# Kernel optimization log

Measured on AMD Instinct MI355X. Metric: run time of the kernel, lower is better.

Reference implementation:

```python
import jax, jax.numpy as jnp
import numpy as np
from jax import lax

S = 512          # IMAGE_SIZE
NP = 11          # num parts (num_layers)
B = 4            # batch_size (hard-coded in original)
FEAT = 9 * 126 * 126  # fc1 in-features: 9*(((S-4)//2-2)//2)**2

_DRAW_ORDER_BIAS = [
    [0.848048096156426, -0.5299192642332049, -0.06623990802915061, 0.5299192642332049, 0.848048096156426, 0.10600601201955324],
    [0.9986295347545738, 0.05233595624294379, -0.001158806553435294, -0.05233595624294379, 0.9986295347545738, -0.022375972781727708],
    [0.8290375725550417, -0.5591929034707469, 0.2758348051438573, 0.5591929034707469, 0.8290375725550417, -0.3679706692738145],
    [0.898794046299167, -0.4383711467890774, -0.1455594743327377, 0.4383711467890774, 0.898794046299167, -0.0037996949408528533],
    [0.7431448254773944, -0.6691306063588581, -0.04191544748895007, 0.6691306063588581, 0.7431448254773944, -0.4385935274816633],
    [0.984807753012208, 0.17364817766693036, 0.09489218227886641, -0.17364817766693036, 0.984807753012208, 0.204382434413116],
    [0.754709580222772, 0.6560590289905073, 0.34755260971666235, -0.6560590289905073, 0.754709580222772, 0.3941816342013059],
    [0.992546151641322, 0.12186934340514749, 0.2294707093902736, -0.12186934340514749, 0.992546151641322, 0.42009272589950425],
    [0.766044443118978, 0.6427876096865394, 0.3722248189351549, -0.6427876096865394, 0.766044443118978, -0.02028262460152125],
    [0.9993908270190958, -0.03489949670250096, -0.16002611816129286, 0.03489949670250096, 0.9993908270190958, 0.3825967914560618],
    [0.9961946980917455, 0.08715574274765818, -0.2047079583082938, -0.08715574274765818, 0.9961946980917455, 0.15872754699051406],
]
CANON_BIAS = np.asarray(_DRAW_ORDER_BIAS, dtype=np.float32).reshape(-1)  # [66]


def setup_inputs() -> dict:
    key = jax.random.key(0)
    ks = jax.random.split(key, 8)
    x = jax.random.uniform(ks[0], (B, (NP + 1) * S, S, 4), dtype=jnp.float32)
    return {
        "x": x,
        "conv1_w": jax.random.normal(ks[1], (7, 4, 5, 5), jnp.float32) * 0.05,
        "conv1_b": jnp.zeros((7,), jnp.float32),
        "conv2_w": jax.random.normal(ks[2], (9, 7, 3, 3), jnp.float32) * 0.05,
        "conv2_b": jnp.zeros((9,), jnp.float32),
        "fc1_w": jax.random.normal(ks[3], (32, FEAT), jnp.float32) * 0.005,
        "fc1_b": jnp.zeros((32,), jnp.float32),
        "fc2_w": jax.random.normal(ks[4], (3 * NP, 32), jnp.float32) * 0.05,
        "fc2_b": jnp.zeros((3 * NP,), jnp.float32),
        "fc3_w": jax.random.normal(ks[5], (6 * NP, 3 * NP), jnp.float32) * 0.01,
        "fc3_b": jnp.asarray(CANON_BIAS),
    }


def _conv_valid(x, w, b):
    y = lax.conv_general_dilated(x, w, (1, 1), 'VALID',
                                 dimension_numbers=('NCHW', 'OIHW', 'NCHW'))
    return y + b[None, :, None, None]


def _maxpool2(x):
    return lax.reduce_window(x, -jnp.inf, lax.max, (1, 1, 2, 2), (1, 1, 2, 2), 'VALID')


def _warp(img, theta):
    """F.affine_grid + F.grid_sample (bilinear, align_corners=False, border pad).
    img: [B,C,S,S], theta: [B,2,3] -> [B,C,S,S]."""
    dt = img.dtype
    coords = (jnp.arange(S, dtype=dt) * 2 + 1) / S - 1  # align_corners=False grid
    xs = coords[None, None, :]   # [1,1,S] varies along W
    ys = coords[None, :, None]   # [1,S,1] varies along H
    gx = theta[:, 0, 0, None, None] * xs + theta[:, 0, 1, None, None] * ys + theta[:, 0, 2, None, None]
    gy = theta[:, 1, 0, None, None] * xs + theta[:, 1, 1, None, None] * ys + theta[:, 1, 2, None, None]
    # unnormalize (align_corners=False)
    ix = ((gx + 1) * S - 1) * 0.5
    iy = ((gy + 1) * S - 1) * 0.5
    x0 = jnp.floor(ix); y0 = jnp.floor(iy)
    wx = (ix - x0)[:, None]; wy = (iy - y0)[:, None]  # [B,1,S,S]
    x0i = jnp.clip(x0.astype(jnp.int32), 0, S - 1)
    x1i = jnp.clip(x0.astype(jnp.int32) + 1, 0, S - 1)
    y0i = jnp.clip(y0.astype(jnp.int32), 0, S - 1)
    y1i = jnp.clip(y0.astype(jnp.int32) + 1, 0, S - 1)
    gather = jax.vmap(lambda im, yi, xi: im[:, yi, xi])  # per-batch [C,S,S]
    v00 = gather(img, y0i, x0i); v01 = gather(img, y0i, x1i)
    v10 = gather(img, y1i, x0i); v11 = gather(img, y1i, x1i)
    return (v00 * (1 - wx) * (1 - wy) + v01 * wx * (1 - wy)
            + v10 * (1 - wx) * wy + v11 * wx * wy)


def reference(x, conv1_w, conv1_b, conv2_w, conv2_b, fc1_w, fc1_b, fc2_w, fc2_b, fc3_w, fc3_b):
    xp = x.transpose(0, 3, 1, 2)                       # [B,4,12S,S]
    chunks = xp.reshape(B, 4, NP + 1, S, S)            # split along H
    loc_in = chunks[:, :, 0]                           # [B,4,S,S]
    parts = chunks[:, :, 1:].transpose(2, 0, 1, 3, 4)  # [NP,B,4,S,S]

    # localization head
    h = _maxpool2(jax.nn.relu(_conv_valid(loc_in, conv1_w, conv1_b)))
    h = _maxpool2(jax.nn.relu(_conv_valid(h, conv2_w, conv2_b)))
    h = h.reshape(B, -1)
    h = jax.nn.relu(h @ fc1_w.T + fc1_b)
    h = jax.nn.relu(h @ fc2_w.T + fc2_b)
    theta = (h @ fc3_w.T + fc3_b).reshape(B, NP, 2, 3)  # [B,NP,2,3]

    Rm = theta[..., :2]                                 # [B,NP,2,2]
    close_to_eye = jnp.einsum('bpij,bpkj->bpik', Rm, Rm).reshape(B, NP, 4)
    translations = theta[..., 2]                        # [B,NP,2]

    warped = jax.vmap(_warp, in_axes=(0, 1))(parts, theta)  # [NP,B,4,S,S]

    stack = warped[0]
    for i in range(1, NP):
        layer = warped[i]
        alpha = jnp.clip(layer[:, -1:], 0.0, 1.0)       # [B,1,S,S]
        stack = jnp.clip(stack - 2 * alpha, -1.0, 1.0)
        stack = jnp.clip(stack + layer + 1.0, -1.0, 1.0)
    return stack, close_to_eye, translations
```

## Files before the change

kernel.cpp:

```cpp
#include <hip/hip_runtime.h>

#define SS 512
#define NPARTS 11
#define NB 4
#define FEAT (9*126*126)

#define H1SZ (4*7*254*254)
#define H2SZ (4*FEAT)
#define OFF_H1 0
#define OFF_H2 (OFF_H1 + H1SZ)
#define OFF_PART (OFF_H2 + H2SZ)
#define OFF_THETA (OFF_PART + 1024)

__global__ __launch_bounds__(256) void conv1_kernel(
    const float4* __restrict__ x4,
    const float* __restrict__ w,
    const float* __restrict__ bias,
    float* __restrict__ h1) {
  __shared__ float4 wlds[175];
  int tid = threadIdx.x;
  {
    float* wf = (float*)wlds;
    for (int i = tid; i < 700; i += 256) {
      int tap = i / 28, r = i % 28;
      int k = r >> 2, c = r & 3;
      int dy = tap / 5, dx = tap % 5;
      wf[i] = w[((k * 4 + c) * 5 + dy) * 5 + dx];
    }
  }
  __syncthreads();

  int b = blockIdx.y;
  int by = blockIdx.x >> 4, bx = blockIdx.x & 15;
  int ty = tid >> 4, tx = tid & 15;
  int py = by * 16 + ty, px = bx * 16 + tx;
  if (py >= 254 || px >= 254) return;

  const float4* img = x4 + (size_t)b * 6144 * 512 + (size_t)(2 * py) * 512 + 2 * px;

  float acc[4][7];
#pragma unroll
  for (int p = 0; p < 4; p++)
#pragma unroll
    for (int k = 0; k < 7; k++) acc[p][k] = bias[k];

#pragma unroll 1
  for (int dy = 0; dy < 5; dy++) {
    const float4* r0 = img + dy * 512;
    const float4* r1 = r0 + 512;
    float4 a0[6], a1[6];
#pragma unroll
    for (int j = 0; j < 6; j++) { a0[j] = r0[j]; a1[j] = r1[j]; }
#pragma unroll
    for (int dx = 0; dx < 5; dx++) {
      float4 v00 = a0[dx], v01 = a0[dx + 1];
      float4 v10 = a1[dx], v11 = a1[dx + 1];
      const float4* wp = &wlds[(dy * 5 + dx) * 7];
#pragma unroll
      for (int k = 0; k < 7; k++) {
        float4 wv = wp[k];
        acc[0][k] += v00.x * wv.x + v00.y * wv.y + v00.z * wv.z + v00.w * wv.w;
        acc[1][k] += v01.x * wv.x + v01.y * wv.y + v01.z * wv.z + v01.w * wv.w;
        acc[2][k] += v10.x * wv.x + v10.y * wv.y + v10.z * wv.z + v10.w * wv.w;
        acc[3][k] += v11.x * wv.x + v11.y * wv.y + v11.z * wv.z + v11.w * wv.w;
      }
    }
  }

#pragma unroll
  for (int k = 0; k < 7; k++) {
    float m = fmaxf(fmaxf(acc[0][k], acc[1][k]), fmaxf(acc[2][k], acc[3][k]));
    h1[(((size_t)b * 7 + k) * 254 + py) * 254 + px] = fmaxf(m, 0.0f);
  }
}

__global__ __launch_bounds__(256) void conv2_kernel(
    const float* __restrict__ h1,
    const float* __restrict__ w,
    const float* __restrict__ bias,
    float* __restrict__ h2) {
  __shared__ float tile[7 * 34 * 35];
  int tid = threadIdx.x;
  int b = blockIdx.y;
  int by = blockIdx.x >> 3, bx = blockIdx.x & 7;
  int y0 = by * 32, x0 = bx * 32;

  for (int i = tid; i < 7 * 34 * 34; i += 256) {
    int c = i / (34 * 34), rem = i % (34 * 34);
    int r = rem / 34, col = rem % 34;
    int gy = y0 + r, gx = x0 + col;
    float v = 0.f;
    if (gy < 254 && gx < 254)
      v = h1[(((size_t)b * 7 + c) * 254 + gy) * 254 + gx];
    tile[(c * 34 + r) * 35 + col] = v;
  }
  __syncthreads();

  int ty = tid >> 4, tx = tid & 15;
  float acc[4][9];
#pragma unroll
  for (int p = 0; p < 4; p++)
#pragma unroll
    for (int k = 0; k < 9; k++) acc[p][k] = bias[k];

  for (int c = 0; c < 7; c++) {
#pragma unroll
    for (int dy = 0; dy < 3; dy++) {
      const float* r0 = &tile[(c * 34 + 2 * ty + dy) * 35 + 2 * tx];
      const float* r1 = r0 + 35;
      float a0[4], a1[4];
#pragma unroll
      for (int j = 0; j < 4; j++) { a0[j] = r0[j]; a1[j] = r1[j]; }
#pragma unroll
      for (int dx = 0; dx < 3; dx++) {
#pragma unroll
        for (int k = 0; k < 9; k++) {
          float wv = w[k * 63 + c * 9 + dy * 3 + dx];
          acc[0][k] += a0[dx] * wv;
          acc[1][k] += a0[dx + 1] * wv;
          acc[2][k] += a1[dx] * wv;
          acc[3][k] += a1[dx + 1] * wv;
        }
      }
    }
  }

  int py = by * 16 + ty, px = bx * 16 + tx;
  if (py < 126 && px < 126) {
#pragma unroll
    for (int k = 0; k < 9; k++) {
      float m = fmaxf(fmaxf(acc[0][k], acc[1][k]), fmaxf(acc[2][k], acc[3][k]));
      h2[(((size_t)b * 9 + k) * 126 + py) * 126 + px] = fmaxf(m, 0.0f);
    }
  }
}

__global__ __launch_bounds__(256) void fc1_kernel(
    const float* __restrict__ h2,
    const float* __restrict__ w,
    float* __restrict__ partials) {
  int j = blockIdx.x;
  int s = blockIdx.y;
  int tid = threadIdx.x;
  const int CH = (FEAT + 7) / 8;
  int f0 = s * CH;
  int f1 = f0 + CH; if (f1 > FEAT) f1 = FEAT;
  float a0 = 0.f, a1 = 0.f, a2 = 0.f, a3 = 0.f;
  const float* wj = w + (size_t)j * FEAT;
  for (int f = f0 + tid; f < f1; f += 256) {
    float wv = wj[f];
    a0 += wv * h2[f];
    a1 += wv * h2[FEAT + f];
    a2 += wv * h2[2 * FEAT + f];
    a3 += wv * h2[3 * FEAT + f];
  }
  __shared__ float4 red[256];
  red[tid] = make_float4(a0, a1, a2, a3);
  __syncthreads();
  for (int off = 128; off > 0; off >>= 1) {
    if (tid < off) {
      float4 o = red[tid + off];
      red[tid].x += o.x; red[tid].y += o.y; red[tid].z += o.z; red[tid].w += o.w;
    }
    __syncthreads();
  }
  if (tid == 0) {
    float4 r = red[0];
    float* p = partials + ((size_t)j * 8 + s) * 4;
    p[0] = r.x; p[1] = r.y; p[2] = r.z; p[3] = r.w;
  }
}

__global__ __launch_bounds__(256) void head_kernel(
    const float* __restrict__ partials,
    const float* __restrict__ b1,
    const float* __restrict__ w2,
    const float* __restrict__ b2,
    const float* __restrict__ w3,
    const float* __restrict__ b3,
    float* __restrict__ theta_out,
    float* __restrict__ out_tail) {
  __shared__ float h32[128];
  __shared__ float h33[132];
  __shared__ float th[264];
  int tid = threadIdx.x;
  for (int t = tid; t < 128; t += 256) {
    int b = t >> 5, j = t & 31;
    float sacc = b1[j];
    for (int k = 0; k < 8; k++) sacc += partials[((size_t)j * 8 + k) * 4 + b];
    h32[b * 32 + j] = fmaxf(sacc, 0.0f);
  }
  __syncthreads();
  for (int t = tid; t < 132; t += 256) {
    int b = t / 33, j2 = t % 33;
    float sacc = b2[j2];
    for (int j = 0; j < 32; j++) sacc += h32[b * 32 + j] * w2[j2 * 32 + j];
    h33[b * 33 + j2] = fmaxf(sacc, 0.0f);
  }
  __syncthreads();
  for (int t = tid; t < 264; t += 256) {
    int b = t / 66, u = t % 66;
    float sacc = b3[u];
    for (int j2 = 0; j2 < 33; j2++) sacc += h33[b * 33 + j2] * w3[u * 33 + j2];
    th[t] = sacc;
    theta_out[t] = sacc;
  }
  __syncthreads();
  for (int t = tid; t < 176; t += 256) {
    int b = t / 44, r = t % 44, p = r / 4, ik = r % 4;
    int i = ik >> 1, k = ik & 1;
    const float* T = &th[b * 66 + p * 6];
    out_tail[t] = T[i * 3 + 0] * T[k * 3 + 0] + T[i * 3 + 1] * T[k * 3 + 1];
  }
  for (int t = tid; t < 88; t += 256) {
    int b = t / 22, r = t % 22, p = r / 2, i = r % 2;
    out_tail[176 + t] = th[b * 66 + p * 6 + i * 3 + 2];
  }
}

__global__ __launch_bounds__(256) void warp_kernel(
    const float4* __restrict__ x4,
    const float* __restrict__ theta,
    float* __restrict__ out) {
  int bid = blockIdx.x;
  int swz = (bid & 7) * 512 + (bid >> 3);
  int b = swz >> 10;
  int t = swz & 1023;
  int ty = t >> 5, tx = t & 31;
  int tid = threadIdx.x;
  int wv = tid >> 6, l = tid & 63;
  int y = ty * 16 + wv * 4 + (l >> 4);
  int x = tx * 16 + (l & 15);

  __shared__ float th[66];
  if (tid < 66) th[tid] = theta[b * 66 + tid];
  __syncthreads();

  const float4* img0 = x4 + (size_t)b * 6144 * 512 + 262144;
  float fx = (float)x, fy = (float)y;
  const float cn = (1.0f / 512.0f) - 1.0f;

  float4 v00, v01, v10, v11;
  float wx, wy;
  {
    float T0 = th[0], T1 = th[1], T2 = th[2];
    float T3 = th[3], T4 = th[4], T5 = th[5];
    float Cx = 256.0f * ((T0 + T1) * cn + T2) + 255.5f;
    float Cy = 256.0f * ((T3 + T4) * cn + T5) + 255.5f;
    float ix = fmaf(T0, fx, fmaf(T1, fy, Cx));
    float iy = fmaf(T3, fx, fmaf(T4, fy, Cy));
    float xf = floorf(ix), yf = floorf(iy);
    wx = ix - xf; wy = iy - yf;
    int x0i = min(max((int)xf, 0), 511);
    int x1i = min(max((int)xf + 1, 0), 511);
    int y0i = min(max((int)yf, 0), 511);
    int y1i = min(max((int)yf + 1, 0), 511);
    int off00 = y0i * 512 + x0i;
    int dxs = x1i - x0i, dys = (y1i - y0i) * 512;
    v00 = img0[off00];
    v01 = img0[off00 + dxs];
    v10 = img0[off00 + dys];
    v11 = img0[off00 + dys + dxs];
  }

  float4 stack = make_float4(0.f, 0.f, 0.f, 0.f);
#pragma unroll 1
  for (int i = 0; i < NPARTS; i++) {
    float cwx = wx, cwy = wy;
    float4 c00 = v00, c01 = v01, c10 = v10, c11 = v11;
    if (i + 1 < NPARTS) {
      float T0 = th[(i + 1) * 6 + 0], T1 = th[(i + 1) * 6 + 1], T2 = th[(i + 1) * 6 + 2];
      float T3 = th[(i + 1) * 6 + 3], T4 = th[(i + 1) * 6 + 4], T5 = th[(i + 1) * 6 + 5];
      float Cx = 256.0f * ((T0 + T1) * cn + T2) + 255.5f;
      float Cy = 256.0f * ((T3 + T4) * cn + T5) + 255.5f;
      float ix = fmaf(T0, fx, fmaf(T1, fy, Cx));
      float iy = fmaf(T3, fx, fmaf(T4, fy, Cy));
      float xf = floorf(ix), yf = floorf(iy);
      wx = ix - xf; wy = iy - yf;
      int x0i = min(max((int)xf, 0), 511);
      int x1i = min(max((int)xf + 1, 0), 511);
      int y0i = min(max((int)yf, 0), 511);
      int y1i = min(max((int)yf + 1, 0), 511);
      int off00 = y0i * 512 + x0i;
      int dxs = x1i - x0i, dys = (y1i - y0i) * 512;
      const float4* img = img0 + (size_t)(i + 1) * 262144;
      v00 = img[off00];
      v01 = img[off00 + dxs];
      v10 = img[off00 + dys];
      v11 = img[off00 + dys + dxs];
    }
    float w00 = (1.f - cwx) * (1.f - cwy), w01 = cwx * (1.f - cwy);
    float w10 = (1.f - cwx) * cwy, w11 = cwx * cwy;
    float4 val;
    val.x = c00.x * w00 + c01.x * w01 + c10.x * w10 + c11.x * w11;
    val.y = c00.y * w00 + c01.y * w01 + c10.y * w10 + c11.y * w11;
    val.z = c00.z * w00 + c01.z * w01 + c10.z * w10 + c11.z * w11;
    val.w = c00.w * w00 + c01.w * w01 + c10.w * w10 + c11.w * w11;
    if (i == 0) {
      stack = val;
    } else {
      float a = fminf(fmaxf(val.w, 0.0f), 1.0f);
      stack.x = fminf(fmaxf(stack.x - 2.f * a, -1.f), 1.f);
      stack.y = fminf(fmaxf(stack.y - 2.f * a, -1.f), 1.f);
      stack.z = fminf(fmaxf(stack.z - 2.f * a, -1.f), 1.f);
      stack.w = fminf(fmaxf(stack.w - 2.f * a, -1.f), 1.f);
      stack.x = fminf(fmaxf(stack.x + val.x + 1.f, -1.f), 1.f);
      stack.y = fminf(fmaxf(stack.y + val.y + 1.f, -1.f), 1.f);
      stack.z = fminf(fmaxf(stack.z + val.z + 1.f, -1.f), 1.f);
      stack.w = fminf(fmaxf(stack.w + val.w + 1.f, -1.f), 1.f);
    }
  }
  size_t obase = (size_t)b * 4 * 262144 + (size_t)y * 512 + x;
  out[obase] = stack.x;
  out[obase + 262144] = stack.y;
  out[obase + 2 * 262144] = stack.z;
  out[obase + 3 * 262144] = stack.w;
}

extern "C" void kernel_launch(void* const* d_in, const int* in_sizes, int n_in,
                              void* d_out, int out_size, void* d_ws, size_t ws_size,
                              hipStream_t stream) {
  const float4* x4 = (const float4*)d_in[0];
  const float* conv1_w = (const float*)d_in[1];
  const float* conv1_b = (const float*)d_in[2];
  const float* conv2_w = (const float*)d_in[3];
  const float* conv2_b = (const float*)d_in[4];
  const float* fc1_w = (const float*)d_in[5];
  const float* fc1_b = (const float*)d_in[6];
  const float* fc2_w = (const float*)d_in[7];
  const float* fc2_b = (const float*)d_in[8];
  const float* fc3_w = (const float*)d_in[9];
  const float* fc3_b = (const float*)d_in[10];
  float* ws = (float*)d_ws;
  float* out = (float*)d_out;

  conv1_kernel<<<dim3(256, 4), 256, 0, stream>>>(x4, conv1_w, conv1_b, ws + OFF_H1);
  conv2_kernel<<<dim3(64, 4), 256, 0, stream>>>(ws + OFF_H1, conv2_w, conv2_b, ws + OFF_H2);
  fc1_kernel<<<dim3(32, 8), 256, 0, stream>>>(ws + OFF_H2, fc1_w, ws + OFF_PART);
  head_kernel<<<1, 256, 0, stream>>>(ws + OFF_PART, fc1_b, fc2_w, fc2_b, fc3_w, fc3_b,
                                     ws + OFF_THETA, out + 4194304);
  warp_kernel<<<4096, 256, 0, stream>>>(x4, ws + OFF_THETA, out);
}
```

Measured before the change: 137.1 us.

## Fuse fc1 into conv2 epilogue and fold MLP head into warp kernel

Conv2 now computes fc1 partial dot products directly from its register outputs, reducing across waves and writing per-block partials, so the h2 intermediate is never stored and re-read. The separate fc1 and head kernels are removed. Each warp block recomputes the small fc2/fc3 head for its own batch from the partials, and block 0 writes the auxiliary outputs. This saves two launches and a round trip through global memory, but it adds redundant per-block head computation in the warp kernel, a serial 32-iteration shuffle-reduction loop in conv2, and a 4x larger fc1 weight read since each batch reads the weights separately.

```diff
diff --git a/kernel.cpp b/kernel.cpp
--- a/kernel.cpp
+++ b/kernel.cpp
@@ -6,11 +6,8 @@
 #define FEAT (9*126*126)
 
 #define H1SZ (4*7*254*254)
-#define H2SZ (4*FEAT)
 #define OFF_H1 0
-#define OFF_H2 (OFF_H1 + H1SZ)
-#define OFF_PART (OFF_H2 + H2SZ)
-#define OFF_THETA (OFF_PART + 1024)
+#define OFF_PART (OFF_H1 + H1SZ)
 
 __global__ __launch_bounds__(256) void conv1_kernel(
     const float4* __restrict__ x4,
@@ -74,15 +71,18 @@
   }
 }
 
-__global__ __launch_bounds__(256) void conv2_kernel(
+__global__ __launch_bounds__(256) void conv2fc1_kernel(
     const float* __restrict__ h1,
     const float* __restrict__ w,
     const float* __restrict__ bias,
-    float* __restrict__ h2) {
+    const float* __restrict__ fw,
+    float* __restrict__ partials) {
   __shared__ float tile[7 * 34 * 35];
+  __shared__ float red[4][32];
   int tid = threadIdx.x;
   int b = blockIdx.y;
-  int by = blockIdx.x >> 3, bx = blockIdx.x & 7;
+  int blkx = blockIdx.x;
+  int by = blkx >> 3, bx = blkx & 7;
   int y0 = by * 32, x0 = bx * 32;
 
   for (int i = tid; i < 7 * 34 * 34; i += 256) {
@@ -126,101 +126,41 @@
   }
 
   int py = by * 16 + ty, px = bx * 16 + tx;
-  if (py < 126 && px < 126) {
-#pragma unroll
-    for (int k = 0; k < 9; k++) {
-      float m = fmaxf(fmaxf(acc[0][k], acc[1][k]), fmaxf(acc[2][k], acc[3][k]));
-      h2[(((size_t)b * 9 + k) * 126 + py) * 126 + px] = fmaxf(m, 0.0f);
-    }
+  bool valid = (py < 126 && px < 126);
+  float hv[9];
+#pragma unroll
+  for (int k = 0; k < 9; k++) {
+    float m = fmaxf(fmaxf(acc[0][k], acc[1][k]), fmaxf(acc[2][k], acc[3][k]));
+    hv[k] = valid ? fmaxf(m, 0.0f) : 0.0f;
+  }
+  int fbase = valid ? (py * 126 + px) : 0;
+
+  int lane = tid & 63, wv = tid >> 6;
+#pragma unroll 1
+  for (int j = 0; j < 32; j++) {
+    const float* wj = fw + (size_t)j * FEAT + fbase;
+    float s = hv[0] * wj[0];
+#pragma unroll
+    for (int k = 1; k < 9; k++) s += hv[k] * wj[k * 15876];
+#pragma unroll
+    for (int off = 32; off > 0; off >>= 1) s += __shfl_down(s, off);
+    if (lane == 0) red[wv][j] = s;
+  }
+  __syncthreads();
+  if (tid < 32) {
+    float s = red[0][tid] + red[1][tid] + red[2][tid] + red[3][tid];
+    partials[((size_t)b * 64 + blkx) * 32 + tid] = s;
   }
 }
 
-__global__ __launch_bounds__(256) void fc1_kernel(
-    const float* __restrict__ h2,
-    const float* __restrict__ w,
-    float* __restrict__ partials) {
-  int j = blockIdx.x;
-  int s = blockIdx.y;
-  int tid = threadIdx.x;
-  const int CH = (FEAT + 7) / 8;
-  int f0 = s * CH;
-  int f1 = f0 + CH; if (f1 > FEAT) f1 = FEAT;
-  float a0 = 0.f, a1 = 0.f, a2 = 0.f, a3 = 0.f;
-  const float* wj = w + (size_t)j * FEAT;
-  for (int f = f0 + tid; f < f1; f += 256) {
-    float wv = wj[f];
-    a0 += wv * h2[f];
-    a1 += wv * h2[FEAT + f];
-    a2 += wv * h2[2 * FEAT + f];
-    a3 += wv * h2[3 * FEAT + f];
-  }
-  __shared__ float4 red[256];
-  red[tid] = make_float4(a0, a1, a2, a3);
-  __syncthreads();
-  for (int off = 128; off > 0; off >>= 1) {
-    if (tid < off) {
-      float4 o = red[tid + off];
-      red[tid].x += o.x; red[tid].y += o.y; red[tid].z += o.z; red[tid].w += o.w;
-    }
-    __syncthreads();
-  }
-  if (tid == 0) {
-    float4 r = red[0];
-    float* p = partials + ((size_t)j * 8 + s) * 4;
-    p[0] = r.x; p[1] = r.y; p[2] = r.z; p[3] = r.w;
-  }
-}
-
-__global__ __launch_bounds__(256) void head_kernel(
+__global__ __launch_bounds__(256) void warp_kernel(
+    const float4* __restrict__ x4,
     const float* __restrict__ partials,
     const float* __restrict__ b1,
     const float* __restrict__ w2,
     const float* __restrict__ b2,
     const float* __restrict__ w3,
     const float* __restrict__ b3,
-    float* __restrict__ theta_out,
-    float* __restrict__ out_tail) {
-  __shared__ float h32[128];
-  __shared__ float h33[132];
-  __shared__ float th[264];
-  int tid = threadIdx.x;
-  for (int t = tid; t < 128; t += 256) {
-    int b = t >> 5, j = t & 31;
-    float sacc = b1[j];
-    for (int k = 0; k < 8; k++) sacc += partials[((size_t)j * 8 + k) * 4 + b];
-    h32[b * 32 + j] = fmaxf(sacc, 0.0f);
-  }
-  __syncthreads();
-  for (int t = tid; t < 132; t += 256) {
-    int b = t / 33, j2 = t % 33;
-    float sacc = b2[j2];
-    for (int j = 0; j < 32; j++) sacc += h32[b * 32 + j] * w2[j2 * 32 + j];
-    h33[b * 33 + j2] = fmaxf(sacc, 0.0f);
-  }
-  __syncthreads();
-  for (int t = tid; t < 264; t += 256) {
-    int b = t / 66, u = t % 66;
-    float sacc = b3[u];
-    for (int j2 = 0; j2 < 33; j2++) sacc += h33[b * 33 + j2] * w3[u * 33 + j2];
-    th[t] = sacc;
-    theta_out[t] = sacc;
-  }
-  __syncthreads();
-  for (int t = tid; t < 176; t += 256) {
-    int b = t / 44, r = t % 44, p = r / 4, ik = r % 4;
-    int i = ik >> 1, k = ik & 1;
-    const float* T = &th[b * 66 + p * 6];
-    out_tail[t] = T[i * 3 + 0] * T[k * 3 + 0] + T[i * 3 + 1] * T[k * 3 + 1];
-  }
-  for (int t = tid; t < 88; t += 256) {
-    int b = t / 22, r = t % 22, p = r / 2, i = r % 2;
-    out_tail[176 + t] = th[b * 66 + p * 6 + i * 3 + 2];
-  }
-}
-
-__global__ __launch_bounds__(256) void warp_kernel(
-    const float4* __restrict__ x4,
-    const float* __restrict__ theta,
     float* __restrict__ out) {
   int bid = blockIdx.x;
   int swz = (bid & 7) * 512 + (bid >> 3);
@@ -228,14 +168,68 @@
   int t = swz & 1023;
   int ty = t >> 5, tx = t & 31;
   int tid = threadIdx.x;
-  int wv = tid >> 6, l = tid & 63;
-  int y = ty * 16 + wv * 4 + (l >> 4);
+
+  __shared__ float h32[32], h33[33], th[66];
+  if (tid < 32) {
+    float s = b1[tid];
+    const float* pb = partials + (size_t)b * 64 * 32 + tid;
+    for (int blk = 0; blk < 64; blk++) s += pb[blk * 32];
+    h32[tid] = fmaxf(s, 0.0f);
+  }
+  __syncthreads();
+  if (tid < 33) {
+    float s = b2[tid];
+    for (int j = 0; j < 32; j++) s += h32[j] * w2[tid * 32 + j];
+    h33[tid] = fmaxf(s, 0.0f);
+  }
+  __syncthreads();
+  if (tid < 66) {
+    float s = b3[tid];
+    for (int j2 = 0; j2 < 33; j2++) s += h33[j2] * w3[tid * 33 + j2];
+    th[tid] = s;
+  }
+  __syncthreads();
+
+  if (bid == 0) {
+    __shared__ float h32b[128], h33b[132], thb[264];
+    for (int u = tid; u < 128; u += 256) {
+      int bb = u >> 5, j = u & 31;
+      float s = b1[j];
+      const float* pb = partials + (size_t)bb * 64 * 32 + j;
+      for (int blk = 0; blk < 64; blk++) s += pb[blk * 32];
+      h32b[u] = fmaxf(s, 0.0f);
+    }
+    __syncthreads();
+    for (int u = tid; u < 132; u += 256) {
+      int bb = u / 33, j2 = u % 33;
+      float s = b2[j2];
+      for (int j = 0; j < 32; j++) s += h32b[bb * 32 + j] * w2[j2 * 32 + j];
+      h33b[u] = fmaxf(s, 0.0f);
+    }
+    __syncthreads();
+    for (int u = tid; u < 264; u += 256) {
+      int bb = u / 66, v = u % 66;
+      float s = b3[v];
+      for (int j2 = 0; j2 < 33; j2++) s += h33b[bb * 33 + j2] * w3[v * 33 + j2];
+      thb[u] = s;
+    }
+    __syncthreads();
+    float* out_tail = out + 4194304;
+    for (int u = tid; u < 176; u += 256) {
+      int bb = u / 44, r = u % 44, p = r / 4, ik = r % 4;
+      int i = ik >> 1, k = ik & 1;
+      const float* T = &thb[bb * 66 + p * 6];
+      out_tail[u] = T[i * 3 + 0] * T[k * 3 + 0] + T[i * 3 + 1] * T[k * 3 + 1];
+    }
+    for (int u = tid; u < 88; u += 256) {
+      int bb = u / 22, r = u % 22, p = r / 2, i = r % 2;
+      out_tail[176 + u] = thb[bb * 66 + p * 6 + i * 3 + 2];
+    }
+  }
+
+  int wvi = tid >> 6, l = tid & 63;
+  int y = ty * 16 + wvi * 4 + (l >> 4);
   int x = tx * 16 + (l & 15);
-
-  __shared__ float th[66];
-  if (tid < 66) th[tid] = theta[b * 66 + tid];
-  __syncthreads();
-
   const float4* img0 = x4 + (size_t)b * 6144 * 512 + 262144;
   float fx = (float)x, fy = (float)y;
   const float cn = (1.0f / 512.0f) - 1.0f;
@@ -335,9 +329,8 @@
   float* out = (float*)d_out;
 
   conv1_kernel<<<dim3(256, 4), 256, 0, stream>>>(x4, conv1_w, conv1_b, ws + OFF_H1);
-  conv2_kernel<<<dim3(64, 4), 256, 0, stream>>>(ws + OFF_H1, conv2_w, conv2_b, ws + OFF_H2);
-  fc1_kernel<<<dim3(32, 8), 256, 0, stream>>>(ws + OFF_H2, fc1_w, ws + OFF_PART);
-  head_kernel<<<1, 256, 0, stream>>>(ws + OFF_PART, fc1_b, fc2_w, fc2_b, fc3_w, fc3_b,
-                                     ws + OFF_THETA, out + 4194304);
-  warp_kernel<<<4096, 256, 0, stream>>>(x4, ws + OFF_THETA, out);
+  conv2fc1_kernel<<<dim3(64, 4), 256, 0, stream>>>(ws + OFF_H1, conv2_w, conv2_b,
+                                                   fc1_w, ws + OFF_PART);
+  warp_kernel<<<4096, 256, 0, stream>>>(x4, ws + OFF_PART, fc1_b, fc2_w, fc2_b,
+                                        fc3_w, fc3_b, out);
 }
```

After: 138.0 us. About the same (+0.7%).
